# Performance work log

Measured on AMD Instinct MI355X. Metric: run time of the kernel, lower is better.

## Reference

```python
import jax, jax.numpy as jnp
import numpy as np

B, G, P, C = 16, 14, 16, 3          # batch, patch grid (14x14), patch size, channels
D, DI, HM, L = 384, 768, 1536, 12   # embed_dim, d_inner=expand*D, mlp_hidden=4*D, depth


def _ln(x, g, b, eps=1e-5):
    m = x.mean(-1, keepdims=True)
    v = ((x - m) ** 2).mean(-1, keepdims=True)
    return (x - m) * jax.lax.rsqrt(v + eps) * g + b


def _lin_attn(seq, wi, bi, wo, bo, g, b):
    # LinearAttention fallback: gated pointwise MLP (SiLU(z)*sigmoid(gate)) + LN + proj_out
    zg = seq @ wi + bi
    z, gate = jnp.split(zg, 2, axis=-1)
    z = jax.nn.silu(z) * jax.nn.sigmoid(gate)
    return _ln(z, g, b) @ wo + bo


def setup_inputs():
    key = jax.random.key(0)
    ks = jax.random.split(key, 8)
    def w(k, shape, s=0.02):
        return (jax.random.normal(k, shape) * s).astype(jnp.float32)
    return {
        'x': jax.random.normal(ks[0], (B, C, G * P, G * P), jnp.float32),
        'patch_w': w(ks[1], (C * P * P, D)), 'patch_b': jnp.zeros((D,), jnp.float32),
        'pe_g': jnp.ones((D,), jnp.float32), 'pe_b': jnp.zeros((D,), jnp.float32),
        'pos': w(ks[2], (1, G * G, D)),
        'n1_g': jnp.ones((L, D), jnp.float32), 'n1_b': jnp.zeros((L, D), jnp.float32),
        'pi_w': w(ks[3], (L, 4, D, 2 * DI)), 'pi_b': jnp.zeros((L, 4, 2 * DI), jnp.float32),
        'po_w': w(ks[4], (L, 4, DI, D)), 'po_b': jnp.zeros((L, 4, D), jnp.float32),
        'la_g': jnp.ones((L, 4, DI), jnp.float32), 'la_b': jnp.zeros((L, 4, DI), jnp.float32),
        'mg_w': w(ks[5], (L, 4 * D, D)), 'mg_b': jnp.zeros((L, D), jnp.float32),
        'sn_g': jnp.ones((L, D), jnp.float32), 'sn_b': jnp.zeros((L, D), jnp.float32),
        'n2_g': jnp.ones((L, D), jnp.float32), 'n2_b': jnp.zeros((L, D), jnp.float32),
        'm1_w': w(ks[6], (L, D, HM)), 'm1_b': jnp.zeros((L, HM), jnp.float32),
        'm2_w': w(ks[7], (L, HM, D)), 'm2_b': jnp.zeros((L, D), jnp.float32),
        'fin_g': jnp.ones((D,), jnp.float32), 'fin_b': jnp.zeros((D,), jnp.float32),
    }


def reference(x, patch_w, patch_b, pe_g, pe_b, pos, n1_g, n1_b, pi_w, pi_b, po_w, po_b,
              la_g, la_b, mg_w, mg_b, sn_g, sn_b, n2_g, n2_b, m1_w, m1_b, m2_w, m2_b,
              fin_g, fin_b):
    Bsz = x.shape[0]
    # Patch embed: non-overlapping conv == per-patch linear projection
    patches = x.reshape(Bsz, C, G, P, G, P).transpose(0, 2, 4, 1, 3, 5).reshape(Bsz, G, G, C * P * P)
    h = _ln(patches @ patch_w + patch_b, pe_g, pe_b)          # [B, G, G, D]
    h = (h.reshape(Bsz, G * G, D) + pos).reshape(Bsz, G, G, D)  # pos embed (no interp: grid==base)
    for l in range(L):
        hn = _ln(h, n1_g[l], n1_b[l])
        # 4-direction scan sequences (-> <- down up)
        ht = hn.transpose(0, 2, 1, 3)
        seqs = [hn.reshape(Bsz, G * G, D),
                hn[:, ::-1, ::-1].reshape(Bsz, G * G, D),
                ht.reshape(Bsz, G * G, D),
                ht[:, ::-1, ::-1].reshape(Bsz, G * G, D)]
        outs = []
        for i in range(4):
            o = _lin_attn(seqs[i], pi_w[l, i], pi_b[l, i], po_w[l, i], po_b[l, i], la_g[l, i], la_b[l, i])
            if i == 1:
                o = o[:, ::-1]
            elif i == 2:
                o = o.reshape(Bsz, G, G, D).transpose(0, 2, 1, 3).reshape(Bsz, G * G, D)
            elif i == 3:
                o = o[:, ::-1].reshape(Bsz, G, G, D).transpose(0, 2, 1, 3).reshape(Bsz, G * G, D)
            outs.append(o)
        merged = jnp.concatenate(outs, axis=-1) @ mg_w[l] + mg_b[l]
        merged = _ln(merged, sn_g[l], sn_b[l]).reshape(Bsz, G, G, D)
        h = h + merged
        hn2 = _ln(h, n2_g[l], n2_b[l])
        h = h + (jax.nn.gelu(hn2 @ m1_w[l] + m1_b[l], approximate=False) @ m2_w[l] + m2_b[l])
    return _ln(h.reshape(Bsz, G * G, D), fin_g, fin_b)  # dense features [B, N, D]
```

## Files before the change

### kernel.cpp

```cpp
#include <hip/hip_runtime.h>
#include <math.h>

typedef unsigned short u16;
typedef __bf16 bf16x8 __attribute__((ext_vector_type(8)));
typedef float f32x4 __attribute__((ext_vector_type(4)));

#define L_   12
#define NTOK 3136
#define MP   3200

__device__ __forceinline__ float b2f(u16 v){ return __builtin_bit_cast(float, (unsigned)v<<16); }
__device__ __forceinline__ u16 f2b(float f){
    unsigned u = __builtin_bit_cast(unsigned, f);
    u += 0x7fffu + ((u>>16)&1u);
    return (u16)(u>>16);
}
__device__ __forceinline__ float wsum(float v){
    #pragma unroll
    for (int o=32;o;o>>=1) v += __shfl_xor(v,o);
    return v;
}
__device__ __forceinline__ void gl_lds16(const void* g, void* l){
    __builtin_amdgcn_global_load_lds(
        (const __attribute__((address_space(1))) void*)g,
        (__attribute__((address_space(3))) void*)l, 16, 0, 0);
}

__device__ __host__ __forceinline__ int rho16(int c){
    return (c < 768) ? (((c>>4)<<5) + (c&15)) : ((((c-768)>>4)<<5) + 16 + ((c-768)&15));
}

__global__ __launch_bounds__(256) void k_transpose(const float* __restrict__ src,
                                                   u16* __restrict__ dst, int R, int C){
    __shared__ float t[32][33];
    long long base = (long long)blockIdx.z * R * C;
    int c0 = blockIdx.x<<5, r0 = blockIdx.y<<5;
    int tx = threadIdx.x & 31, ty = threadIdx.x >> 5;
    #pragma unroll
    for (int i=0;i<32;i+=8)
        t[ty+i][tx] = src[base + (long long)(r0+ty+i)*C + c0 + tx];
    __syncthreads();
    #pragma unroll
    for (int i=0;i<32;i+=8)
        dst[base + (long long)(c0+ty+i)*R + r0 + tx] = f2b(t[tx][ty+i]);
}

__global__ __launch_bounds__(256) void k_transpose_pi(const float* __restrict__ src,
                                                      u16* __restrict__ dst){
    const int R = 384, C = 1536;
    __shared__ float t[32][33];
    long long base = (long long)blockIdx.z * R * C;
    int c0 = blockIdx.x<<5, r0 = blockIdx.y<<5;
    int tx = threadIdx.x & 31, ty = threadIdx.x >> 5;
    #pragma unroll
    for (int i=0;i<32;i+=8)
        t[ty+i][tx] = src[base + (long long)(r0+ty+i)*C + c0 + tx];
    __syncthreads();
    #pragma unroll
    for (int i=0;i<32;i+=8){
        int c = c0 + ty + i;
        dst[base + (long long)rho16(c)*R + r0 + tx] = f2b(t[tx][ty+i]);
    }
}

__global__ __launch_bounds__(256) void k_bi(const float* __restrict__ pi_b, float* __restrict__ out){
    int idx = blockIdx.x*256 + threadIdx.x;
    if (idx >= 48*1536) return;
    int slab = idx / 1536, c = idx - slab*1536;
    int l = slab >> 2, dir = slab & 3;
    out[(long long)l*6144 + dir*1536 + rho16(c)] = pi_b[idx];
}

__global__ __launch_bounds__(384) void k_cvt_bw(const float* __restrict__ po_w,
                                                const float* __restrict__ la_g,
                                                const float* __restrict__ la_b,
                                                u16* __restrict__ po_bf,
                                                float* __restrict__ tvec){
    int z = blockIdx.x, chunk = blockIdx.y;
    int i = threadIdx.x;
    const float* pw = po_w + (long long)z*294912;
    u16* ob = po_bf + (long long)z*294912;
    const float* lb = la_b + (long long)z*768;
    const float* lg = la_g + (long long)z*768;
    float s = 0.f;
    int c0 = chunk*128;
    for (int ci=c0; ci<c0+128; ci++){
        float v = pw[(long long)ci*384 + i];
        s = fmaf(lb[ci], v, s);
        ob[(long long)ci*384 + i] = f2b(v * lg[ci]);
    }
    atomicAdd(tvec + (long long)z*384 + i, s);
}

__global__ __launch_bounds__(384) void k_bw2(const float* __restrict__ tvec,
                                             const float* __restrict__ po_b,
                                             const float* __restrict__ mg_w,
                                             float* __restrict__ fullb){
    int z = blockIdx.x, chunk = blockIdx.y;
    int l = z>>2, dir = z&3;
    int i = threadIdx.x;
    const float* mw = mg_w + (long long)l*589824 + (long long)dir*147456;
    const float* tv = tvec + (long long)z*384;
    const float* pb = po_b + (long long)z*384;
    float s = 0.f;
    int m0 = chunk*64;
    for (int m=m0; m<m0+64; m++) s = fmaf(tv[m]+pb[m], mw[(long long)m*384 + i], s);
    atomicAdd(fullb + (long long)l*384 + i, s);
}

__global__ __launch_bounds__(256) void k_stats(const u16* __restrict__ gated,
                                               float* __restrict__ st){
    int unit = blockIdx.x*4 + (threadIdx.x>>6);
    int lane = threadIdx.x & 63;
    const u16* p = gated + (long long)(unit>>2)*3072 + (unit&3)*768;
    float s1 = 0.f, s2 = 0.f;
    #pragma unroll
    for (int i=0;i<3;i++){
        ushort4 v = *reinterpret_cast<const ushort4*>(p + i*256 + lane*4);
        const u16* a = (const u16*)&v;
        #pragma unroll
        for (int q=0;q<4;q++){ float f = b2f(a[q]); s1 += f; s2 += f*f; }
    }
    s1 = wsum(s1); s2 = wsum(s2);
    if (lane==0){
        st[(long long)unit*2]   = s1;
        st[(long long)unit*2+1] = s2;
    }
}

__global__ __launch_bounds__(256) void k_patches(const float* __restrict__ x, u16* __restrict__ out){
    int idx = blockIdx.x*256 + threadIdx.x;
    int row = idx / 768, col = idx - row*768;
    float v = 0.f;
    if (row < NTOK){
        int b = row / 196, t = row - b*196;
        int gi = t / 14, gj = t - gi*14;
        int c = col >> 8, rem = col & 255, pi = rem >> 4, pj = rem & 15;
        v = x[((long long)(b*3 + c)*224 + gi*16 + pi)*224 + gj*16 + pj];
    }
    out[idx] = f2b(v);
}

template<int EPI, int BM, int BN>
__global__ __launch_bounds__(256) void gemm_tn(
    const u16* __restrict__ A, int lda, long long aSh, long long aSl,
    const u16* __restrict__ Bt, int ldb, long long bSh, long long bSl,
    const float* __restrict__ bias, long long biasSh, int splitBias,
    void* __restrict__ Cbase, int ldc, long long cSh, long long cSl,
    int K, int zshift, const float* __restrict__ aux, float* __restrict__ auxw)
{
    constexpr int AI = BM/32;
    constexpr int BI = BN/32;
    constexpr int NF = (BM==128) ? BN/32 : BN/64;
    int z = blockIdx.z;
    int zh = z >> zshift, zl = z - (zh << zshift);
    const u16* Az  = A  + zh*aSh + zl*aSl;
    const u16* Btz = Bt + zh*bSh + zl*bSl;
    bool addb = bias && (!splitBias || zl == 0);
    long long cOff = zh*cSh + zl*cSl;
    int m0 = blockIdx.y*BM, n0 = blockIdx.x*BN;

    __shared__ u16 As[BM*64];
    __shared__ u16 Bs[BN*64];

    int tid = threadIdx.x;
    int lane = tid & 63;
    int w = tid >> 6;
    int wrb = (BM==128) ? (w>>1)*64 : 0;
    int wcb = (BM==128) ? (w&1)*(BN/2) : w*(BN/4);
    int rsub = lane >> 3, csub = lane & 7;
    int scol = ((csub ^ rsub) << 3);
    int kxor = (lane & 7) << 4;

    const u16* ga[AI]; const u16* gb[BI]; int loa[AI], lob[BI];
    #pragma unroll
    for (int j=0;j<AI;j++){
        int r = j*32 + w*8 + rsub;
        ga[j] = Az + (long long)(m0 + r)*lda + scol;
        loa[j] = (j*32 + w*8)*64;
    }
    #pragma unroll
    for (int j=0;j<BI;j++){
        int r = j*32 + w*8 + rsub;
        gb[j] = Btz + (long long)(n0 + r)*ldb + scol;
        lob[j] = (j*32 + w*8)*64;
    }

    f32x4 acc[4][NF];
    #pragma unroll
    for (int m=0;m<4;m++)
        #pragma unroll
        for (int n=0;n<NF;n++) acc[m][n] = (f32x4){0.f,0.f,0.f,0.f};

    int nkt = K >> 6;

    auto stage = [&](int ko){
        #pragma unroll
        for (int j=0;j<AI;j++) gl_lds16(ga[j] + ko, &As[loa[j]]);
        #pragma unroll
        for (int j=0;j<BI;j++) gl_lds16(gb[j] + ko, &Bs[lob[j]]);
    };

    stage(0);

    for (int kt=0; kt<nkt; ++kt){
        asm volatile("s_waitcnt vmcnt(0)" ::: "memory");
        __builtin_amdgcn_s_barrier();
        const char* as = (const char*)As;
        const char* bs = (const char*)Bs;
        bf16x8 af[2][4], bfr[2][NF];
        #pragma unroll
        for (int kk=0; kk<2; ++kk){
            int kb = ((kk*32 + ((lane>>4)<<3))*2) ^ kxor;
            #pragma unroll
            for (int m=0;m<4;m++){
                int r = wrb + m*16 + (lane&15);
                af[kk][m] = *reinterpret_cast<const bf16x8*>(as + r*128 + kb);
            }
            #pragma unroll
            for (int n=0;n<NF;n++){
                int r = wcb + n*16 + (lane&15);
                bfr[kk][n] = *reinterpret_cast<const bf16x8*>(bs + r*128 + kb);
            }
        }
        asm volatile("s_waitcnt lgkmcnt(0)" ::: "memory");
        __builtin_amdgcn_sched_barrier(0);
        __builtin_amdgcn_s_barrier();
        if (kt+1 < nkt) stage((kt+1)<<6);
        #pragma unroll
        for (int kk=0; kk<2; ++kk)
            #pragma unroll
            for (int m=0;m<4;m++)
                #pragma unroll
                for (int n=0;n<NF;n++)
                    acc[m][n] = __builtin_amdgcn_mfma_f32_16x16x32_bf16(af[kk][m], bfr[kk][n], acc[m][n], 0,0,0);
    }

    int rbase = m0 + wrb;
    int nbase = n0 + wcb;
    if (EPI==3){
        int dir = n0/1536;
        #pragma unroll
        for (int np2=0; np2<NF/2; ++np2){
            int ncz = nbase + (np2*2)*16 + (lane&15);
            int pz  = ncz - dir*1536;
            int ci  = ((pz>>5)<<4) + (pz&15);
            float bz = addb ? bias[ncz]      : 0.f;
            float bg = addb ? bias[ncz+16]   : 0.f;
            #pragma unroll
            for (int m=0;m<4;m++){
                #pragma unroll
                for (int r4=0;r4<4;r4++){
                    int row = rbase + m*16 + ((lane>>4)<<2) + r4;
                    float vz = acc[m][np2*2][r4]   + bz;
                    float vg = acc[m][np2*2+1][r4] + bg;
                    float gv = vz / ((1.f+__expf(-vz))*(1.f+__expf(-vg)));
                    ((u16*)Cbase)[(long long)row*3072 + dir*768 + ci] = f2b(gv);
                }
            }
        }
    } else if (EPI==4){
        #pragma unroll
        for (int m=0;m<4;m++){
            #pragma unroll
            for (int r4=0;r4<4;r4++){
                int row = rbase + m*16 + ((lane>>4)<<2) + r4;
                float st1 = aux[((long long)row*4 + zl)*2];
                float st2 = aux[((long long)row*4 + zl)*2 + 1];
                float mu = st1*(1.f/768.f);
                float rs = rsqrtf(st2*(1.f/768.f) - mu*mu + 1e-5f);
                #pragma unroll
                for (int n=0;n<NF;n++){
                    int ncol = nbase + n*16 + (lane&15);
                    float gsv = bias[(long long)zl*384 + ncol];
                    ((float*)Cbase)[(long long)row*ldc + ncol + cOff] = (acc[m][n][r4] - mu*gsv)*rs;
                }
            }
        }
    } else if (EPI==5){
        #pragma unroll
        for (int m=0;m<4;m++){
            #pragma unroll
            for (int r4=0;r4<4;r4++){
                int row = rbase + m*16 + ((lane>>4)<<2) + r4;
                float s = 0.f;
                #pragma unroll
                for (int n=0;n<NF;n++){
                    int ncol = nbase + n*16 + (lane&15);
                    u16 rv = f2b(acc[m][n][r4]);
                    ((u16*)Cbase)[(long long)row*ldc + ncol + cOff] = rv;
                    s += b2f(rv);
                }
                #pragma unroll
                for (int o=1;o<16;o<<=1) s += __shfl_xor(s, o);
                if ((lane&15)==0) atomicAdd(auxw + (long long)z*384 + row, s);
            }
        }
    } else {
        #pragma unroll
        for (int m=0;m<4;m++){
            #pragma unroll
            for (int n=0;n<NF;n++){
                int ncol = nbase + n*16 + (lane&15);
                float bv = addb ? bias[zh*biasSh + ncol] : 0.f;
                #pragma unroll
                for (int r4=0;r4<4;r4++){
                    int row = rbase + m*16 + ((lane>>4)<<2) + r4;
                    float v = acc[m][n][r4] + bv;
                    long long idx = (long long)row*ldc + ncol + cOff;
                    if (EPI==0)      ((u16*)Cbase)[idx] = f2b(v);
                    else if (EPI==1){
                        float gl = 0.5f*v*(1.f + erff(v*0.70710678118f));
                        ((u16*)Cbase)[idx] = f2b(gl);
                    }
                    else             ((float*)Cbase)[idx] = v;
                }
            }
        }
    }
}

template<int MODE>
__global__ __launch_bounds__(256) void k_addln(float* __restrict__ h,
        const float* __restrict__ parts, int np,
        const float* __restrict__ g, const float* __restrict__ b, void* __restrict__ out){
    int row = blockIdx.x*4 + (threadIdx.x>>6);
    int lane = threadIdx.x & 63;
    float* hp = h + (long long)row*384;
    float v[6]; float s = 0.f;
    #pragma unroll
    for (int i=0;i<6;i++){
        int c = lane + i*64;
        float t = hp[c];
        for (int p=0;p<np;p++) t += parts[(long long)p*MP*384 + (long long)row*384 + c];
        v[i] = t; s += t;
    }
    if (MODE==0 && np){
        #pragma unroll
        for (int i=0;i<6;i++) hp[lane + i*64] = v[i];
    }
    float mu = wsum(s)*(1.f/384.f);
    float q = 0.f;
    #pragma unroll
    for (int i=0;i<6;i++){ float d = v[i]-mu; q += d*d; }
    float rs = rsqrtf(wsum(q)*(1.f/384.f) + 1e-5f);
    if (MODE==0){
        u16* op = (u16*)out + (long long)row*384;
        #pragma unroll
        for (int i=0;i<6;i++){ int c = lane + i*64; op[c] = f2b((v[i]-mu)*rs*g[c] + b[c]); }
    } else {
        float* op = (float*)out + (long long)row*384;
        #pragma unroll
        for (int i=0;i<6;i++){ int c = lane + i*64; op[c] = (v[i]-mu)*rs*g[c] + b[c]; }
    }
}

__global__ __launch_bounds__(256) void k_pe_ln(const float* __restrict__ parts,
        const float* __restrict__ g, const float* __restrict__ b,
        const float* __restrict__ pos, float* __restrict__ h,
        const float* __restrict__ n1g, const float* __restrict__ n1b,
        u16* __restrict__ hn){
    int row = blockIdx.x*4 + (threadIdx.x>>6);
    int lane = threadIdx.x & 63;
    float v[6]; float s = 0.f;
    #pragma unroll
    for (int i=0;i<6;i++){
        int c = lane + i*64;
        float t = parts[(long long)row*384 + c] + parts[(long long)MP*384 + (long long)row*384 + c];
        v[i] = t; s += t;
    }
    float mu = wsum(s)*(1.f/384.f);
    float q = 0.f;
    #pragma unroll
    for (int i=0;i<6;i++){ float d = v[i]-mu; q += d*d; }
    float rs = rsqrtf(wsum(q)*(1.f/384.f) + 1e-5f);
    int t = row % 196;
    const float* pp = pos + (long long)t*384;
    float* op = h + (long long)row*384;
    float hv[6]; float s2 = 0.f;
    #pragma unroll
    for (int i=0;i<6;i++){
        int c = lane + i*64;
        float nv = (v[i]-mu)*rs*g[c] + b[c] + pp[c];
        op[c] = nv; hv[i] = nv; s2 += nv;
    }
    float mu2 = wsum(s2)*(1.f/384.f);
    float q2 = 0.f;
    #pragma unroll
    for (int i=0;i<6;i++){ float d = hv[i]-mu2; q2 += d*d; }
    float rs2 = rsqrtf(wsum(q2)*(1.f/384.f) + 1e-5f);
    u16* hp = hn + (long long)row*384;
    #pragma unroll
    for (int i=0;i<6;i++){ int c = lane + i*64; hp[c] = f2b((hv[i]-mu2)*rs2*n1g[c] + n1b[c]); }
}

__global__ __launch_bounds__(256) void k_sn_ln(const float* __restrict__ parts,
        const float* __restrict__ fullb, const float* __restrict__ mgb,
        const float* __restrict__ sg, const float* __restrict__ sb,
        float* __restrict__ h,
        const float* __restrict__ n2g, const float* __restrict__ n2b,
        u16* __restrict__ hn2){
    int row = blockIdx.x*4 + (threadIdx.x>>6);
    int lane = threadIdx.x & 63;
    float v[6]; float s = 0.f;
    #pragma unroll
    for (int i=0;i<6;i++){
        int c = lane + i*64;
        long long o = (long long)row*384 + c;
        float t = mgb[c] + fullb[c];
        #pragma unroll
        for (int p=0;p<4;p++) t += parts[(long long)p*MP*384 + o];
        v[i] = t; s += t;
    }
    float mu = wsum(s)*(1.f/384.f);
    float q = 0.f;
    #pragma unroll
    for (int i=0;i<6;i++){ float d = v[i]-mu; q += d*d; }
    float rs = rsqrtf(wsum(q)*(1.f/384.f) + 1e-5f);
    float* hp = h + (long long)row*384;
    float hv[6]; float s2 = 0.f;
    #pragma unroll
    for (int i=0;i<6;i++){
        int c = lane + i*64;
        float nv = hp[c] + (v[i]-mu)*rs*sg[c] + sb[c];
        hp[c] = nv; hv[i] = nv; s2 += nv;
    }
    float mu2 = wsum(s2)*(1.f/384.f);
    float q2 = 0.f;
    #pragma unroll
    for (int i=0;i<6;i++){ float d = hv[i]-mu2; q2 += d*d; }
    float rs2 = rsqrtf(wsum(q2)*(1.f/384.f) + 1e-5f);
    u16* op = hn2 + (long long)row*384;
    #pragma unroll
    for (int i=0;i<6;i++){ int c = lane + i*64; op[c] = f2b((hv[i]-mu2)*rs2*n2g[c] + n2b[c]); }
}

extern "C" void kernel_launch(void* const* d_in, const int* in_sizes, int n_in,
                              void* d_out, int out_size, void* d_ws, size_t ws_size,
                              hipStream_t stream)
{
    const float* x      = (const float*)d_in[0];
    const float* patch_w= (const float*)d_in[1];
    const float* patch_b= (const float*)d_in[2];
    const float* pe_g   = (const float*)d_in[3];
    const float* pe_b   = (const float*)d_in[4];
    const float* pos    = (const float*)d_in[5];
    const float* n1_g   = (const float*)d_in[6];
    const float* n1_b   = (const float*)d_in[7];
    const float* pi_w   = (const float*)d_in[8];
    const float* pi_b   = (const float*)d_in[9];
    const float* po_w   = (const float*)d_in[10];
    const float* po_b   = (const float*)d_in[11];
    const float* la_g   = (const float*)d_in[12];
    const float* la_b   = (const float*)d_in[13];
    const float* mg_w   = (const float*)d_in[14];
    const float* mg_b   = (const float*)d_in[15];
    const float* sn_g   = (const float*)d_in[16];
    const float* sn_b   = (const float*)d_in[17];
    const float* n2_g   = (const float*)d_in[18];
    const float* n2_b   = (const float*)d_in[19];
    const float* m1_w   = (const float*)d_in[20];
    const float* m1_b   = (const float*)d_in[21];
    const float* m2_w   = (const float*)d_in[22];
    const float* m2_b   = (const float*)d_in[23];
    const float* fin_g  = (const float*)d_in[24];
    const float* fin_b  = (const float*)d_in[25];

    char* wptr = (char*)d_ws;
    auto carve = [&](long long elems, int esz)->void*{
        void* p = (void*)wptr;
        wptr += ((elems*(long long)esz + 255)/256)*256;
        return p;
    };

    u16* wt_pi  = (u16*)carve(28311552, 2);
    u16* wt_mgr = (u16*)carve(7077888, 2);
    u16* wt_m1  = (u16*)carve(7077888, 2);
    u16* wt_m2  = (u16*)carve(7077888, 2);
    u16* wt_pe  = (u16*)carve(294912, 2);
    u16* po_bf  = (u16*)carve(14155776, 2);
    u16* WcT    = (u16*)carve(14155776, 2);
    float* Gs   = (float*)carve(48*384, 4);
    float* tvec = (float*)carve(48*384, 4);
    float* fullb= (float*)carve(12*384, 4);
    size_t zbytes = (size_t)((char*)(fullb + 12*384) - (char*)Gs);
    float* stats= (float*)carve(MP*8, 4);
    float* pib_i= (float*)carve(12*6144, 4);
    float* h    = (float*)carve((long long)MP*384, 4);
    float* parts= (float*)carve(4LL*MP*384, 4);
    u16* patches= (u16*)carve((long long)MP*768, 2);
    u16* hn     = (u16*)carve((long long)MP*384, 2);
    u16* gated  = (u16*)carve((long long)MP*3072, 2);
    u16* outs   = (u16*)carve((long long)MP*1536, 2);

    dim3 blk(256);

    hipMemsetAsync(Gs, 0, zbytes, stream);
    k_transpose_pi<<<dim3(48,12,48), blk, 0, stream>>>(pi_w, wt_pi);
    k_bi<<<dim3((48*1536+255)/256), blk, 0, stream>>>(pi_b, pib_i);
    k_transpose<<<dim3(12,12,48), blk, 0, stream>>>(mg_w,   wt_mgr, 384, 384);
    k_transpose<<<dim3(48,12,12), blk, 0, stream>>>(m1_w,   wt_m1, 384, 1536);
    k_transpose<<<dim3(12,48,12), blk, 0, stream>>>(m2_w,   wt_m2, 1536, 384);
    k_transpose<<<dim3(12,24,1),  blk, 0, stream>>>(patch_w,wt_pe, 768, 384);
    k_cvt_bw<<<dim3(48,6), dim3(384), 0, stream>>>(po_w, la_g, la_b, po_bf, tvec);
    k_bw2<<<dim3(48,6), dim3(384), 0, stream>>>(tvec, po_b, mg_w, fullb);
    gemm_tn<5,128,128><<<dim3(6,3,48), blk, 0, stream>>>(
        wt_mgr, 384, 589824LL, 147456LL,
        po_bf,  384, 1179648LL, 294912LL,
        nullptr, 0, 0,
        WcT, 3072, 1179648LL, 768LL, 384, 2, nullptr, Gs);

    k_patches<<<dim3(MP*768/256), blk, 0, stream>>>(x, patches);
    gemm_tn<2,64,128><<<dim3(3,50,2), blk, 0, stream>>>(
        patches, 768, 0, 384,
        wt_pe,   768, 0, 384,
        patch_b, 0, 1,
        parts, 384, 0, (long long)MP*384, 384, 1, nullptr, nullptr);
    k_pe_ln<<<dim3(MP/4), blk, 0, stream>>>(parts, pe_g, pe_b, pos, h, n1_g, n1_b, hn);

    for (int l=0; l<L_; ++l){
        gemm_tn<3,128,128><<<dim3(48,25,1), blk, 0, stream>>>(
            hn, 384, 0, 0,
            wt_pi + (long long)l*2359296, 384, 0, 0,
            pib_i + (long long)l*6144, 0, 0,
            gated, 3072, 0, 0, 384, 0, nullptr, nullptr);
        k_stats<<<dim3(MP), blk, 0, stream>>>(gated, stats);
        gemm_tn<4,64,128><<<dim3(3,50,4), blk, 0, stream>>>(
            gated, 3072, 0, 768,
            WcT + (long long)l*1179648, 3072, 0, 768,
            Gs + (long long)l*1536, 0, 0,
            parts, 384, 0, (long long)MP*384, 768, 2, stats, nullptr);
        k_sn_ln<<<dim3(MP/4), blk, 0, stream>>>(parts,
                                                fullb + (long long)l*384, mg_b + l*384,
                                                sn_g + l*384, sn_b + l*384,
                                                h, n2_g + l*384, n2_b + l*384, hn);
        gemm_tn<1,64,128><<<dim3(12,50,1), blk, 0, stream>>>(
            hn, 384, 0, 0,
            wt_m1 + (long long)l*589824, 384, 0, 0,
            m1_b + (long long)l*1536, 0, 0,
            outs, 1536, 0, 0, 384, 0, nullptr, nullptr);
        gemm_tn<2,64,128><<<dim3(3,50,2), blk, 0, stream>>>(
            outs, 1536, 0, 768,
            wt_m2 + (long long)l*589824, 1536, 0, 768,
            m2_b + l*384, 0, 1,
            parts, 384, 0, (long long)MP*384, 768, 1, nullptr, nullptr);
        if (l < L_-1)
            k_addln<0><<<dim3(MP/4), blk, 0, stream>>>(h, parts, 2,
                n1_g + (l+1)*384, n1_b + (l+1)*384, hn);
        else
            k_addln<1><<<dim3(NTOK/4), blk, 0, stream>>>(h, parts, 2,
                fin_g, fin_b, (float*)d_out);
    }
}
```

Before: 1.258 ms.

## Fuse LayerNorm statistics into gated GEMM epilogue, drop separate stats kernel

The separate k_stats kernel, which re-read the bf16 gated tensor to compute per-row, per-direction sums and sums of squares, is removed. The gated projection GEMM epilogue now reduces partial sums across 16 lanes and writes per-64-column partials. The downstream GEMM reduces those 24 partials per row into shared memory at block start, giving mean and rstd. This saves one kernel launch per layer and a full read of the gated activation, at the cost of extra shuffles in the epilogue and statistics taken from fp32 values rather than the rounded bf16 values.

```diff
diff --git a/kernel.cpp b/kernel.cpp
--- a/kernel.cpp
+++ b/kernel.cpp
@@ -106,26 +106,6 @@
     int m0 = chunk*64;
     for (int m=m0; m<m0+64; m++) s = fmaf(tv[m]+pb[m], mw[(long long)m*384 + i], s);
     atomicAdd(fullb + (long long)l*384 + i, s);
-}
-
-__global__ __launch_bounds__(256) void k_stats(const u16* __restrict__ gated,
-                                               float* __restrict__ st){
-    int unit = blockIdx.x*4 + (threadIdx.x>>6);
-    int lane = threadIdx.x & 63;
-    const u16* p = gated + (long long)(unit>>2)*3072 + (unit&3)*768;
-    float s1 = 0.f, s2 = 0.f;
-    #pragma unroll
-    for (int i=0;i<3;i++){
-        ushort4 v = *reinterpret_cast<const ushort4*>(p + i*256 + lane*4);
-        const u16* a = (const u16*)&v;
-        #pragma unroll
-        for (int q=0;q<4;q++){ float f = b2f(a[q]); s1 += f; s2 += f*f; }
-    }
-    s1 = wsum(s1); s2 = wsum(s2);
-    if (lane==0){
-        st[(long long)unit*2]   = s1;
-        st[(long long)unit*2+1] = s2;
-    }
 }
 
 __global__ __launch_bounds__(256) void k_patches(const float* __restrict__ x, u16* __restrict__ out){
@@ -162,6 +142,7 @@
 
     __shared__ u16 As[BM*64];
     __shared__ u16 Bs[BN*64];
+    __shared__ float2 sln[64];
 
     int tid = threadIdx.x;
     int lane = tid & 63;
@@ -171,6 +152,17 @@
     int rsub = lane >> 3, csub = lane & 7;
     int scol = ((csub ^ rsub) << 3);
     int kxor = (lane & 7) << 4;
+
+    if (EPI==4 && tid < 64){
+        const float2* pp = (const float2*)aux;
+        long long base = ((long long)(m0 + tid)*4 + zl)*24;
+        float s1 = 0.f, s2 = 0.f;
+        #pragma unroll
+        for (int c=0;c<24;c++){ float2 v = pp[base + c]; s1 += v.x; s2 += v.y; }
+        float mu = s1*(1.f/768.f);
+        float rs = rsqrtf(s2*(1.f/768.f) - mu*mu + 1e-5f);
+        sln[tid] = make_float2(mu, rs);
+    }
 
     const u16* ga[AI]; const u16* gb[BI]; int loa[AI], lob[BI];
     #pragma unroll
@@ -240,23 +232,34 @@
     int nbase = n0 + wcb;
     if (EPI==3){
         int dir = n0/1536;
+        int sc  = ((n0 - dir*1536) >> 6) + (wcb >> 6);
+        float bzv[NF/2], bgv[NF/2]; int civ[NF/2];
         #pragma unroll
         for (int np2=0; np2<NF/2; ++np2){
             int ncz = nbase + (np2*2)*16 + (lane&15);
             int pz  = ncz - dir*1536;
-            int ci  = ((pz>>5)<<4) + (pz&15);
-            float bz = addb ? bias[ncz]      : 0.f;
-            float bg = addb ? bias[ncz+16]   : 0.f;
-            #pragma unroll
-            for (int m=0;m<4;m++){
-                #pragma unroll
-                for (int r4=0;r4<4;r4++){
-                    int row = rbase + m*16 + ((lane>>4)<<2) + r4;
-                    float vz = acc[m][np2*2][r4]   + bz;
-                    float vg = acc[m][np2*2+1][r4] + bg;
+            civ[np2] = ((pz>>5)<<4) + (pz&15);
+            bzv[np2] = addb ? bias[ncz]    : 0.f;
+            bgv[np2] = addb ? bias[ncz+16] : 0.f;
+        }
+        #pragma unroll
+        for (int m=0;m<4;m++){
+            #pragma unroll
+            for (int r4=0;r4<4;r4++){
+                int row = rbase + m*16 + ((lane>>4)<<2) + r4;
+                float s1 = 0.f, s2 = 0.f;
+                #pragma unroll
+                for (int np2=0; np2<NF/2; ++np2){
+                    float vz = acc[m][np2*2][r4]   + bzv[np2];
+                    float vg = acc[m][np2*2+1][r4] + bgv[np2];
                     float gv = vz / ((1.f+__expf(-vz))*(1.f+__expf(-vg)));
-                    ((u16*)Cbase)[(long long)row*3072 + dir*768 + ci] = f2b(gv);
+                    ((u16*)Cbase)[(long long)row*3072 + dir*768 + civ[np2]] = f2b(gv);
+                    s1 += gv; s2 += gv*gv;
                 }
+                #pragma unroll
+                for (int o=1;o<16;o<<=1){ s1 += __shfl_xor(s1,o); s2 += __shfl_xor(s2,o); }
+                if ((lane&15)==0)
+                    ((float2*)auxw)[((long long)row*4 + dir)*24 + sc] = make_float2(s1, s2);
             }
         }
     } else if (EPI==4){
@@ -264,11 +267,10 @@
         for (int m=0;m<4;m++){
             #pragma unroll
             for (int r4=0;r4<4;r4++){
-                int row = rbase + m*16 + ((lane>>4)<<2) + r4;
-                float st1 = aux[((long long)row*4 + zl)*2];
-                float st2 = aux[((long long)row*4 + zl)*2 + 1];
-                float mu = st1*(1.f/768.f);
-                float rs = rsqrtf(st2*(1.f/768.f) - mu*mu + 1e-5f);
+                int row_l = m*16 + ((lane>>4)<<2) + r4;
+                int row = m0 + row_l;
+                float mu = sln[row_l].x;
+                float rs = sln[row_l].y;
                 #pragma unroll
                 for (int n=0;n<NF;n++){
                     int ncol = nbase + n*16 + (lane&15);
@@ -484,7 +486,7 @@
     float* tvec = (float*)carve(48*384, 4);
     float* fullb= (float*)carve(12*384, 4);
     size_t zbytes = (size_t)((char*)(fullb + 12*384) - (char*)Gs);
-    float* stats= (float*)carve(MP*8, 4);
+    float* pstats=(float*)carve((long long)MP*4*24*2, 4);
     float* pib_i= (float*)carve(12*6144, 4);
     float* h    = (float*)carve((long long)MP*384, 4);
     float* parts= (float*)carve(4LL*MP*384, 4);
@@ -523,13 +525,12 @@
             hn, 384, 0, 0,
             wt_pi + (long long)l*2359296, 384, 0, 0,
             pib_i + (long long)l*6144, 0, 0,
-            gated, 3072, 0, 0, 384, 0, nullptr, nullptr);
-        k_stats<<<dim3(MP), blk, 0, stream>>>(gated, stats);
+            gated, 3072, 0, 0, 384, 0, nullptr, pstats);
         gemm_tn<4,64,128><<<dim3(3,50,4), blk, 0, stream>>>(
             gated, 3072, 0, 768,
             WcT + (long long)l*1179648, 3072, 0, 768,
             Gs + (long long)l*1536, 0, 0,
-            parts, 384, 0, (long long)MP*384, 768, 2, stats, nullptr);
+            parts, 384, 0, (long long)MP*384, 768, 2, pstats, nullptr);
         k_sn_ln<<<dim3(MP/4), blk, 0, stream>>>(parts,
                                                 fullb + (long long)l*384, mg_b + l*384,
                                                 sn_g + l*384, sn_b + l*384,
```

Result: no change. 1.259 ms (+0.1%).
